# Kernel optimization log

Measured on AMD Instinct MI355X. Metric: run time of the kernel, lower is better.

## Reference

```python
import jax, jax.numpy as jnp
import numpy as np

N_NODES = 50000
N_EDGES = 800000


def gcn_conv(x, src, dst, W, b, n):
    # PyG GCNConv: add self-loops, symmetric normalization D^-1/2 (A+I) D^-1/2,
    # linear transform, scatter-add aggregation, then bias.
    loop = jnp.arange(n, dtype=src.dtype)
    src2 = jnp.concatenate([src, loop])
    dst2 = jnp.concatenate([dst, loop])
    deg = jax.ops.segment_sum(jnp.ones(src2.shape[0], x.dtype), dst2, num_segments=n)
    dis = jnp.where(deg > 0, jax.lax.rsqrt(jnp.maximum(deg, 1e-12)), 0.0)
    norm = dis[src2] * dis[dst2]                      # [E+N]
    xw = x @ W                                        # [N, out]
    msg = xw[src2] * norm[:, None]                    # [E+N, out] gather
    out = jax.ops.segment_sum(msg, dst2, num_segments=n)  # scatter-add
    return out + b


def setup_inputs() -> dict:
    key = jax.random.key(0)
    ks = jax.random.split(key, 8)
    d_in, d_h, d_out = 128, 128, 10
    x = jax.random.normal(ks[0], (N_NODES, d_in), dtype=jnp.float32)
    edge_index = jax.random.randint(ks[1], (2, N_EDGES), 0, N_NODES, dtype=jnp.int64)
    s = 1.0 / np.sqrt(d_in)
    W1 = jax.random.normal(ks[2], (d_in, d_h), dtype=jnp.float32) * s
    b1 = jnp.zeros((d_h,), jnp.float32)
    W2 = jax.random.normal(ks[3], (d_h, d_h), dtype=jnp.float32) * s
    b2 = jnp.zeros((d_h,), jnp.float32)
    W3 = jax.random.normal(ks[4], (d_h, d_out), dtype=jnp.float32) * s
    b3 = jnp.zeros((d_out,), jnp.float32)
    return {"x": x, "edge_index": edge_index, "W1": W1, "b1": b1,
            "W2": W2, "b2": b2, "W3": W3, "b3": b3}


def reference(x, edge_index, W1, b1, W2, b2, W3, b3):
    n = x.shape[0]
    src, dst = edge_index[0], edge_index[1]
    h = gcn_conv(x, src, dst, W1, b1, n)
    h = jax.nn.relu(h)
    # dropout(p=0.5) is identity in eval mode (training=False)
    h = gcn_conv(h, src, dst, W2, b2, n)
    h = gcn_conv(h, src, dst, W3, b3, n)
    return jax.nn.log_softmax(h, axis=1)
```

## Files before the change

kernel.cpp:

```cpp
#include <hip/hip_runtime.h>
#include <cstdint>
#include <cstddef>


typedef unsigned int uint;
typedef unsigned short u16;
typedef uint  uint4e  __attribute__((ext_vector_type(4)));
typedef float float4e __attribute__((ext_vector_type(4)));
typedef float float2e __attribute__((ext_vector_type(2)));
typedef uint  uint2e  __attribute__((ext_vector_type(2)));
typedef int   int2e   __attribute__((ext_vector_type(2)));
typedef int   int4e   __attribute__((ext_vector_type(4)));
using bf16x8 = __attribute__((ext_vector_type(8))) short;
using f32x4  = __attribute__((ext_vector_type(4))) float;

__device__ __forceinline__ float bf_lo(uint v) { return __uint_as_float(v << 16); }
__device__ __forceinline__ float bf_hi(uint v) { return __uint_as_float(v & 0xffff0000u); }
__device__ __forceinline__ u16 bf16_1(float a) {
    uint ua = __float_as_uint(a);
    ua = (ua + 0x7fffu + ((ua >> 16) & 1u)) >> 16;
    return (u16)ua;
}
__device__ __forceinline__ uint pack_bf2(float a, float b) {
    return (uint)bf16_1(a) | ((uint)bf16_1(b) << 16);
}

__global__ __launch_bounds__(256) void passA_wt(const int* __restrict__ ei, int E,
        int* __restrict__ cntA, int nbkt, int nca,
        const float* __restrict__ W1, const float* __restrict__ W2,
        const float* __restrict__ W3, const float* __restrict__ b2,
        u16* __restrict__ Wt1, float* __restrict__ W23, float* __restrict__ b23) {
    int tid = threadIdx.x, b = blockIdx.x;
    if (b < nca) {
        __shared__ int h[256];
        h[tid] = 0;
        __syncthreads();
        int ch = (E + nca - 1) / nca;
        int beg = b * ch, end = min(beg + ch, E);
        for (int e = beg + tid; e < end; e += 256)
            atomicAdd(&h[ei[E + e] >> 8], 1);
        __syncthreads();
        if (tid < nbkt) cntA[tid * nca + b] = h[tid];
    } else if (b == nca) {
        for (int i = 0; i < 64; ++i) {
            int idx = tid + i * 256;
            int k = idx >> 7, c = idx & 127;
            Wt1[c * 128 + k] = bf16_1(W1[idx]);
        }
        int c = tid >> 4, j0 = tid & 15;
        float acc = 0.f;
        if (c < 10) {
#pragma unroll
            for (int j = 0; j < 128; j += 16)
                acc += b2[j + j0] * W3[(j + j0) * 10 + c];
        }
#pragma unroll
        for (int m = 1; m < 16; m <<= 1) acc += __shfl_xor(acc, m);
        if (c < 10 && j0 == 0) b23[c] = acc;
    } else {
        __shared__ float w3s[1280];
        for (int i = tid; i < 1280; i += 256) w3s[i] = W3[i];
        __syncthreads();
        int idx = (b - nca - 1) * 256 + tid;
        int k = idx / 10, c = idx % 10;
        const float* w2r = W2 + (size_t)k * 128;
        float a0 = 0.f, a1 = 0.f, a2 = 0.f, a3 = 0.f;
#pragma unroll
        for (int j = 0; j < 128; j += 4) {
            a0 += w2r[j + 0] * w3s[(j + 0) * 10 + c];
            a1 += w2r[j + 1] * w3s[(j + 1) * 10 + c];
            a2 += w2r[j + 2] * w3s[(j + 2) * 10 + c];
            a3 += w2r[j + 3] * w3s[(j + 3) * 10 + c];
        }
        W23[idx] = (a0 + a1) + (a2 + a3);
    }
}

__global__ __launch_bounds__(256) void scan1(int* __restrict__ cntA, int nca,
        int* __restrict__ btot) {
    __shared__ int s[256];
    int b = blockIdx.x, tid = threadIdx.x;
    int v = cntA[b * nca + tid];
    s[tid] = v;
    __syncthreads();
    for (int d = 1; d < 256; d <<= 1) {
        int t = (tid >= d) ? s[tid - d] : 0;
        __syncthreads();
        s[tid] += t;
        __syncthreads();
    }
    cntA[b * nca + tid] = s[tid] - v;
    if (tid == 255) btot[b] = s[255];
}

__global__ __launch_bounds__(256) void passB(const int* __restrict__ ei, int E,
        const int* __restrict__ cntA, int nca, int nbkt,
        const int* __restrict__ btot, int2e* __restrict__ ebkt) {
    __shared__ int sc[256];
    __shared__ int cur[256];
    int tid = threadIdx.x, b = blockIdx.x;
    int v = (tid < nbkt) ? btot[tid] : 0;
    sc[tid] = v;
    __syncthreads();
    for (int d = 1; d < 256; d <<= 1) {
        int t = (tid >= d) ? sc[tid - d] : 0;
        __syncthreads();
        sc[tid] += t;
        __syncthreads();
    }
    cur[tid] = (sc[tid] - v) + ((tid < nbkt) ? cntA[tid * nca + b] : 0);
    __syncthreads();
    int ch = (E + nca - 1) / nca;
    int beg = b * ch, end = min(beg + ch, E);
    int e = beg + tid * 4;
    for (; e + 3 < end; e += 1024) {
        int4e s4 = *reinterpret_cast<const int4e*>(ei + e);
        int4e d4 = *reinterpret_cast<const int4e*>(ei + E + e);
#pragma unroll
        for (int k = 0; k < 4; ++k) {
            int s = k == 0 ? s4.x : k == 1 ? s4.y : k == 2 ? s4.z : s4.w;
            int d = k == 0 ? d4.x : k == 1 ? d4.y : k == 2 ? d4.z : d4.w;
            int pos = atomicAdd(&cur[d >> 8], 1);
            int2e pkt;
            pkt.x = s;
            pkt.y = d;
            ebkt[pos] = pkt;
        }
    }
    for (; e < end; ++e) {
        int s = ei[e], d = ei[E + e];
        int pos = atomicAdd(&cur[d >> 8], 1);
        int2e pkt;
        pkt.x = s;
        pkt.y = d;
        ebkt[pos] = pkt;
    }
}

__global__ __launch_bounds__(256) void passC(const int2e* __restrict__ ebkt,
        const int* __restrict__ btot, int2e* __restrict__ esort,
        int* __restrict__ row_ptr, float* __restrict__ dis, int n, int nbkt, int E) {
    __shared__ int sc[256];
    __shared__ int fc[256];
    __shared__ int s_base;
    int k = blockIdx.x, tid = threadIdx.x;
    int bt = (tid < nbkt) ? btot[tid] : 0;
    sc[tid] = bt;
    __syncthreads();
    for (int d = 1; d < 256; d <<= 1) {
        int t = (tid >= d) ? sc[tid - d] : 0;
        __syncthreads();
        sc[tid] += t;
        __syncthreads();
    }
    if (tid == k) s_base = sc[tid] - bt;
    fc[tid] = 0;
    __syncthreads();
    int base = s_base;
    int endb = base + btot[k];
    int node0 = k << 8;
    for (int i = base + tid; i < endb; i += 256)
        atomicAdd(&fc[ebkt[i].y & 255], 1);
    __syncthreads();
    int v = fc[tid];
    sc[tid] = v;
    __syncthreads();
    for (int d = 1; d < 256; d <<= 1) {
        int t = (tid >= d) ? sc[tid - d] : 0;
        __syncthreads();
        sc[tid] += t;
        __syncthreads();
    }
    int excl = sc[tid] - v;
    if (node0 + tid < n) {
        dis[node0 + tid] = rsqrtf((float)(v + 1));
        row_ptr[node0 + tid] = base + excl;
    }
    __syncthreads();
    fc[tid] = base + excl;
    __syncthreads();
    for (int i = base + tid; i < endb; i += 256) {
        int2e ed = ebkt[i];
        int pos = atomicAdd(&fc[ed.y & 255], 1);
        esort[pos] = ed;
    }
    if (k == 0 && tid == 0) row_ptr[n] = E;
}

__global__ __launch_bounds__(256) void gemm_mfma(const float* __restrict__ A,
        const u16* __restrict__ Wt, u16* __restrict__ out, int n) {
    constexpr int LDA = 136;
    __shared__ u16 as[64 * LDA];
    int tid = threadIdx.x;
    int wave = tid >> 6, lane = tid & 63;
    int row0 = blockIdx.x * 64;
    int l16 = lane & 15;
    int krow = (lane >> 4) * 8;

#pragma unroll
    for (int i = 0; i < 8; ++i) {
        int idx = tid + i * 256;
        int r = idx >> 5;
        int q = (idx & 31) * 4;
        float4e v = {0.f, 0.f, 0.f, 0.f};
        if (row0 + r < n)
            v = *reinterpret_cast<const float4e*>(A + (size_t)(row0 + r) * 128 + q);
        uint2e p;
        p.x = pack_bf2(v.x, v.y);
        p.y = pack_bf2(v.z, v.w);
        *reinterpret_cast<uint2e*>(&as[r * LDA + q]) = p;
    }

    bf16x8 b[2][4];
#pragma unroll
    for (int n2 = 0; n2 < 2; ++n2)
#pragma unroll
        for (int kb = 0; kb < 4; ++kb)
            b[n2][kb] = *reinterpret_cast<const bf16x8*>(
                Wt + (size_t)(wave * 32 + n2 * 16 + l16) * 128 + kb * 32 + krow);

    __syncthreads();

    f32x4 acc[4][2] = {};
#pragma unroll
    for (int m = 0; m < 4; ++m) {
#pragma unroll
        for (int kb = 0; kb < 4; ++kb) {
            bf16x8 a = *reinterpret_cast<const bf16x8*>(
                &as[(m * 16 + l16) * LDA + kb * 32 + krow]);
#pragma unroll
            for (int n2 = 0; n2 < 2; ++n2)
                acc[m][n2] = __builtin_amdgcn_mfma_f32_16x16x32_bf16(a, b[n2][kb], acc[m][n2], 0, 0, 0);
        }
    }

    __syncthreads();
    u16* cs = as;
#pragma unroll
    for (int m = 0; m < 4; ++m) {
        int rb = m * 16 + (lane >> 4) * 4;
#pragma unroll
        for (int n2 = 0; n2 < 2; ++n2) {
            int col = wave * 32 + n2 * 16 + l16;
#pragma unroll
            for (int r = 0; r < 4; ++r)
                cs[(rb + r) * 128 + col] = bf16_1(acc[m][n2][r]);
        }
    }
    __syncthreads();
#pragma unroll
    for (int i = 0; i < 4; ++i) {
        int idx = tid + i * 256;
        int r = idx >> 4;
        int q = (idx & 15) * 8;
        if (row0 + r < n)
            *reinterpret_cast<uint4e*>(out + (size_t)(row0 + r) * 128 + q) =
                *reinterpret_cast<const uint4e*>(&cs[r * 128 + q]);
    }
}

__device__ __forceinline__ void gather_accum(const uint* __restrict__ xw,
        const int2e* __restrict__ esort, const float* __restrict__ dis,
        int v, int lane, int beg, int end, float& ax, float& ay) {
    float dv = dis[v];
    int e = beg;
    for (; e + 7 < end; e += 8) {
        int2e ed[8];
        uint vv[8];
        float wd[8];
#pragma unroll
        for (int j = 0; j < 8; ++j) ed[j] = esort[e + j];
#pragma unroll
        for (int j = 0; j < 8; ++j) {
            vv[j] = xw[(size_t)ed[j].x * 64 + lane];
            wd[j] = dis[ed[j].x];
        }
#pragma unroll
        for (int j = 0; j < 8; ++j) {
            float w = wd[j] * dv;
            ax += w * bf_lo(vv[j]);
            ay += w * bf_hi(vv[j]);
        }
    }
    for (; e + 1 < end; e += 2) {
        int2e e0 = esort[e];
        int2e e1 = esort[e + 1];
        uint v0 = xw[(size_t)e0.x * 64 + lane];
        uint v1 = xw[(size_t)e1.x * 64 + lane];
        float w0 = dis[e0.x] * dv, w1 = dis[e1.x] * dv;
        ax += w0 * bf_lo(v0); ay += w0 * bf_hi(v0);
        ax += w1 * bf_lo(v1); ay += w1 * bf_hi(v1);
    }
    if (e < end) {
        int2e e0 = esort[e];
        uint v0 = xw[(size_t)e0.x * 64 + lane];
        float w0 = dis[e0.x] * dv;
        ax += w0 * bf_lo(v0); ay += w0 * bf_hi(v0);
    }
    float wv = dv * dv;
    uint vs = xw[(size_t)v * 64 + lane];
    ax += wv * bf_lo(vs); ay += wv * bf_hi(vs);
}

__global__ __launch_bounds__(256) void agg_proj_kernel(const uint* __restrict__ xw,
        const int* __restrict__ row_ptr, const int2e* __restrict__ esort,
        const float* __restrict__ dis, const float* __restrict__ b1,
        const float* __restrict__ W23, uint* __restrict__ z, int n) {
    int v = (int)((blockIdx.x * blockDim.x + threadIdx.x) >> 6);
    int lane = threadIdx.x & 63;
    if (v >= n) return;
    float ax = 0.f, ay = 0.f;
    gather_accum(xw, esort, dis, v, lane, row_ptr[v], row_ptr[v + 1], ax, ay);
    ax = fmaxf(ax + b1[lane * 2], 0.f);
    ay = fmaxf(ay + b1[lane * 2 + 1], 0.f);
    const float* w0 = W23 + (size_t)lane * 20;
    float p[10];
#pragma unroll
    for (int c = 0; c < 10; ++c) p[c] = ax * w0[c] + ay * w0[10 + c];
#pragma unroll
    for (int c = 0; c < 10; ++c) {
#pragma unroll
        for (int d = 1; d < 64; d <<= 1) p[c] += __shfl_xor(p[c], d);
    }
    if (lane < 5) z[(size_t)v * 5 + lane] = pack_bf2(p[2 * lane], p[2 * lane + 1]);
}

template <int FINAL>
__global__ __launch_bounds__(256) void agg10_kernel(const uint* __restrict__ zin,
        const int* __restrict__ row_ptr, const int2e* __restrict__ esort,
        const float* __restrict__ dis, const float* __restrict__ b23,
        const float* __restrict__ b3, void* __restrict__ zout, int n) {
    int wid = (int)((blockIdx.x * blockDim.x + threadIdx.x) >> 6);
    int lane = threadIdx.x & 63;
    int grp = lane >> 4, gl = lane & 15;
    int v = wid * 4 + grp;
    bool act = (v < n);
    bool dl = (gl < 5);
    int beg = act ? row_ptr[v] : 0;
    int end = act ? row_ptr[v + 1] : 0;
    float dv = act ? dis[v] : 0.f;
    float ax = 0.f, ay = 0.f, sw = 0.f;
    int e = beg;
    for (; e + 7 < end; e += 8) {
        int2e ed[8];
        uint zz[8];
        float wd[8];
#pragma unroll
        for (int j = 0; j < 8; ++j) ed[j] = esort[e + j];
#pragma unroll
        for (int j = 0; j < 8; ++j) {
            zz[j] = dl ? zin[(size_t)ed[j].x * 5 + gl] : 0u;
            wd[j] = dis[ed[j].x];
        }
#pragma unroll
        for (int j = 0; j < 8; ++j) {
            float w = wd[j] * dv;
            ax += w * bf_lo(zz[j]);
            ay += w * bf_hi(zz[j]);
            sw += w;
        }
    }
    for (; e < end; ++e) {
        int2e e0 = esort[e];
        uint z0 = dl ? zin[(size_t)e0.x * 5 + gl] : 0u;
        float w0 = dis[e0.x] * dv;
        ax += w0 * bf_lo(z0);
        ay += w0 * bf_hi(z0);
        sw += w0;
    }
    if (act) {
        float wv = dv * dv;
        uint zs = dl ? zin[(size_t)v * 5 + gl] : 0u;
        ax += wv * bf_lo(zs);
        ay += wv * bf_hi(zs);
        sw += wv;
    }
    if (FINAL == 0) {
        if (act && dl) ((uint*)zout)[(size_t)v * 5 + gl] = pack_bf2(ax, ay);
    } else {
        float pa = 0.f, pb = 0.f;
        if (dl) {
            pa = ax + sw * b23[2 * gl] + b3[2 * gl];
            pb = ay + sw * b23[2 * gl + 1] + b3[2 * gl + 1];
        }
        float m = dl ? fmaxf(pa, pb) : -3.4e38f;
#pragma unroll
        for (int mask = 1; mask < 16; mask <<= 1) m = fmaxf(m, __shfl_xor(m, mask));
        float s = dl ? (__expf(pa - m) + __expf(pb - m)) : 0.f;
#pragma unroll
        for (int mask = 1; mask < 16; mask <<= 1) s += __shfl_xor(s, mask);
        float ls = __logf(s);
        if (act && dl) {
            float2e o = {pa - m - ls, pb - m - ls};
            *reinterpret_cast<float2e*>((float*)zout + (size_t)v * 10 + 2 * gl) = o;
        }
    }
}

extern "C" void kernel_launch(void* const* d_in, const int* in_sizes, int n_in,
                              void* d_out, int out_size, void* d_ws, size_t ws_size,
                              hipStream_t stream) {
    const float* x  = (const float*)d_in[0];
    const int*   ei = (const int*)d_in[1];
    const float* W1 = (const float*)d_in[2];
    const float* b1 = (const float*)d_in[3];
    const float* W2 = (const float*)d_in[4];
    const float* b2 = (const float*)d_in[5];
    const float* W3 = (const float*)d_in[6];
    const float* b3 = (const float*)d_in[7];
    int N = in_sizes[0] / 128;
    int E = in_sizes[1] / 2;
    int NBKT = (N + 255) >> 8;
    const int NCA = 256;

    char* ws = (char*)d_ws;
    size_t off = 0;
    auto alloc = [&](size_t bytes) -> char* {
        char* p = ws + off;
        off = (off + bytes + 255) & ~(size_t)255;
        return p;
    };
    int*   cntA    = (int*)alloc((size_t)NBKT * NCA * 4);
    int*   btot    = (int*)alloc(256 * 4);
    int*   row_ptr = (int*)alloc(((size_t)N + 1) * 4);
    float* dis     = (float*)alloc((size_t)N * 4);
    u16*   Wt1     = (u16*)alloc(128 * 128 * 2);
    float* W23     = (float*)alloc(128 * 10 * 4);
    float* b23     = (float*)alloc(10 * 4);
    int2e* ebkt    = (int2e*)alloc((size_t)E * 8);
    int2e* esort   = (int2e*)alloc((size_t)E * 8);
    uint*  bufA    = (uint*)alloc((size_t)N * 64 * 4);
    uint*  z       = (uint*)alloc((size_t)N * 5 * 4);
    uint*  z2      = (uint*)alloc((size_t)N * 5 * 4);

    passA_wt<<<NCA + 6, 256, 0, stream>>>(ei, E, cntA, NBKT, NCA, W1, W2, W3, b2,
                                          Wt1, W23, b23);
    gemm_mfma<<<(N + 63) / 64, 256, 0, stream>>>(x, Wt1, (u16*)bufA, N);
    scan1<<<NBKT, 256, 0, stream>>>(cntA, NCA, btot);
    passB<<<NCA, 256, 0, stream>>>(ei, E, cntA, NCA, NBKT, btot, ebkt);
    passC<<<NBKT, 256, 0, stream>>>(ebkt, btot, esort, row_ptr, dis, N, NBKT, E);
    agg_proj_kernel<<<(N + 3) / 4, 256, 0, stream>>>(bufA, row_ptr, esort, dis, b1, W23, z, N);
    agg10_kernel<0><<<(N + 15) / 16, 256, 0, stream>>>(z, row_ptr, esort, dis, nullptr, nullptr, z2, N);
    agg10_kernel<1><<<(N + 15) / 16, 256, 0, stream>>>(z2, row_ptr, esort, dis, b23, b3, d_out, N);
}
```

Baseline: 128.0 us.

## Compress bucketed and sorted edge arrays to 16-bit node indices

Packs each edge's source and destination into one 32-bit word for the bucketing pass. The sorted CSR edge list now stores only a 16-bit source index instead of an 8-byte (src,dst) pair. This cuts memory traffic in the sort passes and in all three aggregation kernels, which read the edge list repeatedly. The encoding assumes node ids fit in 16 bits (N < 65536), and nothing in the code guards that limit.

```diff
diff --git a/kernel.cpp b/kernel.cpp
--- a/kernel.cpp
+++ b/kernel.cpp
@@ -9,7 +9,6 @@
 typedef float float4e __attribute__((ext_vector_type(4)));
 typedef float float2e __attribute__((ext_vector_type(2)));
 typedef uint  uint2e  __attribute__((ext_vector_type(2)));
-typedef int   int2e   __attribute__((ext_vector_type(2)));
 typedef int   int4e   __attribute__((ext_vector_type(4)));
 using bf16x8 = __attribute__((ext_vector_type(8))) short;
 using f32x4  = __attribute__((ext_vector_type(4))) float;
@@ -95,7 +94,7 @@
 
 __global__ __launch_bounds__(256) void passB(const int* __restrict__ ei, int E,
         const int* __restrict__ cntA, int nca, int nbkt,
-        const int* __restrict__ btot, int2e* __restrict__ ebkt) {
+        const int* __restrict__ btot, uint* __restrict__ ebkt) {
     __shared__ int sc[256];
     __shared__ int cur[256];
     int tid = threadIdx.x, b = blockIdx.x;
@@ -121,24 +120,18 @@
             int s = k == 0 ? s4.x : k == 1 ? s4.y : k == 2 ? s4.z : s4.w;
             int d = k == 0 ? d4.x : k == 1 ? d4.y : k == 2 ? d4.z : d4.w;
             int pos = atomicAdd(&cur[d >> 8], 1);
-            int2e pkt;
-            pkt.x = s;
-            pkt.y = d;
-            ebkt[pos] = pkt;
+            ebkt[pos] = ((uint)d << 16) | (uint)s;
         }
     }
     for (; e < end; ++e) {
         int s = ei[e], d = ei[E + e];
         int pos = atomicAdd(&cur[d >> 8], 1);
-        int2e pkt;
-        pkt.x = s;
-        pkt.y = d;
-        ebkt[pos] = pkt;
-    }
-}
-
-__global__ __launch_bounds__(256) void passC(const int2e* __restrict__ ebkt,
-        const int* __restrict__ btot, int2e* __restrict__ esort,
+        ebkt[pos] = ((uint)d << 16) | (uint)s;
+    }
+}
+
+__global__ __launch_bounds__(256) void passC(const uint* __restrict__ ebkt,
+        const int* __restrict__ btot, u16* __restrict__ esort,
         int* __restrict__ row_ptr, float* __restrict__ dis, int n, int nbkt, int E) {
     __shared__ int sc[256];
     __shared__ int fc[256];
@@ -160,7 +153,7 @@
     int endb = base + btot[k];
     int node0 = k << 8;
     for (int i = base + tid; i < endb; i += 256)
-        atomicAdd(&fc[ebkt[i].y & 255], 1);
+        atomicAdd(&fc[(ebkt[i] >> 16) & 255], 1);
     __syncthreads();
     int v = fc[tid];
     sc[tid] = v;
@@ -180,9 +173,9 @@
     fc[tid] = base + excl;
     __syncthreads();
     for (int i = base + tid; i < endb; i += 256) {
-        int2e ed = ebkt[i];
-        int pos = atomicAdd(&fc[ed.y & 255], 1);
-        esort[pos] = ed;
+        uint ed = ebkt[i];
+        int pos = atomicAdd(&fc[(ed >> 16) & 255], 1);
+        esort[pos] = (u16)(ed & 0xffffu);
     }
     if (k == 0 && tid == 0) row_ptr[n] = E;
 }
@@ -260,20 +253,20 @@
 }
 
 __device__ __forceinline__ void gather_accum(const uint* __restrict__ xw,
-        const int2e* __restrict__ esort, const float* __restrict__ dis,
+        const u16* __restrict__ esort, const float* __restrict__ dis,
         int v, int lane, int beg, int end, float& ax, float& ay) {
     float dv = dis[v];
     int e = beg;
     for (; e + 7 < end; e += 8) {
-        int2e ed[8];
+        int sidx[8];
         uint vv[8];
         float wd[8];
 #pragma unroll
-        for (int j = 0; j < 8; ++j) ed[j] = esort[e + j];
+        for (int j = 0; j < 8; ++j) sidx[j] = esort[e + j];
 #pragma unroll
         for (int j = 0; j < 8; ++j) {
-            vv[j] = xw[(size_t)ed[j].x * 64 + lane];
-            wd[j] = dis[ed[j].x];
+            vv[j] = xw[(size_t)sidx[j] * 64 + lane];
+            wd[j] = dis[sidx[j]];
         }
 #pragma unroll
         for (int j = 0; j < 8; ++j) {
@@ -283,18 +276,18 @@
         }
     }
     for (; e + 1 < end; e += 2) {
-        int2e e0 = esort[e];
-        int2e e1 = esort[e + 1];
-        uint v0 = xw[(size_t)e0.x * 64 + lane];
-        uint v1 = xw[(size_t)e1.x * 64 + lane];
-        float w0 = dis[e0.x] * dv, w1 = dis[e1.x] * dv;
+        int s0 = esort[e];
+        int s1 = esort[e + 1];
+        uint v0 = xw[(size_t)s0 * 64 + lane];
+        uint v1 = xw[(size_t)s1 * 64 + lane];
+        float w0 = dis[s0] * dv, w1 = dis[s1] * dv;
         ax += w0 * bf_lo(v0); ay += w0 * bf_hi(v0);
         ax += w1 * bf_lo(v1); ay += w1 * bf_hi(v1);
     }
     if (e < end) {
-        int2e e0 = esort[e];
-        uint v0 = xw[(size_t)e0.x * 64 + lane];
-        float w0 = dis[e0.x] * dv;
+        int s0 = esort[e];
+        uint v0 = xw[(size_t)s0 * 64 + lane];
+        float w0 = dis[s0] * dv;
         ax += w0 * bf_lo(v0); ay += w0 * bf_hi(v0);
     }
     float wv = dv * dv;
@@ -303,7 +296,7 @@
 }
 
 __global__ __launch_bounds__(256) void agg_proj_kernel(const uint* __restrict__ xw,
-        const int* __restrict__ row_ptr, const int2e* __restrict__ esort,
+        const int* __restrict__ row_ptr, const u16* __restrict__ esort,
         const float* __restrict__ dis, const float* __restrict__ b1,
         const float* __restrict__ W23, uint* __restrict__ z, int n) {
     int v = (int)((blockIdx.x * blockDim.x + threadIdx.x) >> 6);
@@ -327,7 +320,7 @@
 
 template <int FINAL>
 __global__ __launch_bounds__(256) void agg10_kernel(const uint* __restrict__ zin,
-        const int* __restrict__ row_ptr, const int2e* __restrict__ esort,
+        const int* __restrict__ row_ptr, const u16* __restrict__ esort,
         const float* __restrict__ dis, const float* __restrict__ b23,
         const float* __restrict__ b3, void* __restrict__ zout, int n) {
     int wid = (int)((blockIdx.x * blockDim.x + threadIdx.x) >> 6);
@@ -342,15 +335,15 @@
     float ax = 0.f, ay = 0.f, sw = 0.f;
     int e = beg;
     for (; e + 7 < end; e += 8) {
-        int2e ed[8];
+        int sidx[8];
         uint zz[8];
         float wd[8];
 #pragma unroll
-        for (int j = 0; j < 8; ++j) ed[j] = esort[e + j];
+        for (int j = 0; j < 8; ++j) sidx[j] = esort[e + j];
 #pragma unroll
         for (int j = 0; j < 8; ++j) {
-            zz[j] = dl ? zin[(size_t)ed[j].x * 5 + gl] : 0u;
-            wd[j] = dis[ed[j].x];
+            zz[j] = dl ? zin[(size_t)sidx[j] * 5 + gl] : 0u;
+            wd[j] = dis[sidx[j]];
         }
 #pragma unroll
         for (int j = 0; j < 8; ++j) {
@@ -361,9 +354,9 @@
         }
     }
     for (; e < end; ++e) {
-        int2e e0 = esort[e];
-        uint z0 = dl ? zin[(size_t)e0.x * 5 + gl] : 0u;
-        float w0 = dis[e0.x] * dv;
+        int s0 = esort[e];
+        uint z0 = dl ? zin[(size_t)s0 * 5 + gl] : 0u;
+        float w0 = dis[s0] * dv;
         ax += w0 * bf_lo(z0);
         ay += w0 * bf_hi(z0);
         sw += w0;
@@ -427,8 +420,8 @@
     u16*   Wt1     = (u16*)alloc(128 * 128 * 2);
     float* W23     = (float*)alloc(128 * 10 * 4);
     float* b23     = (float*)alloc(10 * 4);
-    int2e* ebkt    = (int2e*)alloc((size_t)E * 8);
-    int2e* esort   = (int2e*)alloc((size_t)E * 8);
+    uint*  ebkt    = (uint*)alloc((size_t)E * 4);
+    u16*   esort   = (u16*)alloc((size_t)E * 2);
     uint*  bufA    = (uint*)alloc((size_t)N * 64 * 4);
     uint*  z       = (uint*)alloc((size_t)N * 5 * 4);
     uint*  z2      = (uint*)alloc((size_t)N * 5 * 4);
```

After: 123.5 us. 1.04x faster.
